# Kernel optimization log

Measured on AMD Instinct MI355X. Metric: run time of the kernel, lower is better.

## Reference

```python
import jax, jax.numpy as jnp
import numpy as np

N = 100000
IN_DIM, HID_DIM, EMB_DIM = 128, 64, 32
E = 1600000


def _gcn_conv(x, W, b, src, tgt, n):
    """PyG GCNConv: linear transform, add self-loops, sym-normalized scatter-add.
    W: [in, out], b: [out]. src/tgt: [E'] incl. self-loops handled by caller."""
    h = x @ W  # [n, out] -- transform before propagate (PyG order)
    deg = jax.ops.segment_sum(jnp.ones_like(tgt, dtype=h.dtype), tgt, num_segments=n)
    dinv = jnp.where(deg > 0, jax.lax.rsqrt(deg), 0.0)
    norm = dinv[src] * dinv[tgt]  # [E']
    msgs = h[src] * norm[:, None]  # [E', out]
    out = jax.ops.segment_sum(msgs, tgt, num_segments=n)
    return out + b


def setup_inputs() -> dict:
    key = jax.random.key(0)
    ks = jax.random.split(key, 6)
    x = jax.random.normal(ks[0], (N, IN_DIM), dtype=jnp.float32)
    edge_index = jax.random.randint(ks[1], (2, E), 0, N, dtype=jnp.int64)
    s1 = 1.0 / np.sqrt(IN_DIM)
    s2 = 1.0 / np.sqrt(HID_DIM)
    W1 = jax.random.uniform(ks[2], (IN_DIM, HID_DIM), jnp.float32, -s1, s1)
    b1 = jnp.zeros((HID_DIM,), jnp.float32)
    W2 = jax.random.uniform(ks[3], (HID_DIM, EMB_DIM), jnp.float32, -s2, s2)
    b2 = jnp.zeros((EMB_DIM,), jnp.float32)
    return {"x": x, "W1": W1, "b1": b1, "W2": W2, "b2": b2, "edge_index": edge_index}


def reference(x, W1, b1, W2, b2, edge_index):
    n = x.shape[0]
    src, tgt = edge_index[0], edge_index[1]
    # add self-loops once (same graph used by both convs)
    loops = jnp.arange(n, dtype=edge_index.dtype)
    src_sl = jnp.concatenate([src, loops])
    tgt_sl = jnp.concatenate([tgt, loops])
    h = jax.nn.relu(_gcn_conv(x, W1, b1, src_sl, tgt_sl, n))
    z = _gcn_conv(h, W2, b2, src_sl, tgt_sl, n)  # [n, EMB_DIM]
    # decode on original edges: edge-wise dot product
    recon = jnp.sum(z[src] * z[tgt], axis=1)  # [E]
    return z, recon
```

## Files before the change

### kernel.cpp

```cpp
#include <hip/hip_runtime.h>
#include <hip/hip_fp16.h>
#include <math.h>


#define NBMAX 256
#define BSHIFT 9
#define BNODES 512
#define CH 4096
#define CAPSHIFT 14
#define CAP (1 << CAPSHIFT)

typedef _Float16 half8 __attribute__((ext_vector_type(8)));
typedef float floatx4 __attribute__((ext_vector_type(4)));

static inline int divup(int a, int b) { return (a + b - 1) / b; }

__device__ inline void acc8(__half2* a, float4 v) {
    const __half2* h = (const __half2*)&v;
    a[0] = __hadd2(a[0], h[0]);
    a[1] = __hadd2(a[1], h[1]);
    a[2] = __hadd2(a[2], h[2]);
    a[3] = __hadd2(a[3], h[3]);
}
__device__ inline unsigned short f2bf(float f) {
    unsigned u = __builtin_bit_cast(unsigned, f);
    u = (u + 0x7FFFu + ((u >> 16) & 1u)) >> 16;
    return (unsigned short)u;
}


__global__ void k_init(int* __restrict__ gcur, unsigned* __restrict__ hs_pad,
                       unsigned* __restrict__ zs_pad) {
    int t = threadIdx.x;
    if (t < NBMAX) gcur[t] = t << CAPSHIFT;
    if (t < 32) hs_pad[t] = 0;
    else if (t < 48) zs_pad[t - 32] = 0;
}


__global__ __launch_bounds__(256) void k_part(const int* __restrict__ src,
                                              const int* __restrict__ tgt,
                                              int* __restrict__ gcur,
                                              unsigned* __restrict__ ebuf, int E, int NB) {
    __shared__ int h[NBMAX];
    __shared__ int base[NBMAX];
    int tid = threadIdx.x;
    int e0 = blockIdx.x * CH;
    for (int b = tid; b < NB; b += 256) h[b] = 0;
    __syncthreads();
    unsigned pk[16];
    int sv[16];
#pragma unroll
    for (int r = 0; r < 4; r++) {
        int e = e0 + (r * 256 + tid) * 4;
        if (e + 3 < E) {
            int4 t4 = *(const int4*)(tgt + e);
            int4 s4 = *(const int4*)(src + e);
            int tv[4] = {t4.x, t4.y, t4.z, t4.w};
            int sw[4] = {s4.x, s4.y, s4.z, s4.w};
#pragma unroll
            for (int j = 0; j < 4; j++) {
                int t = tv[j];
                int b = t >> BSHIFT;
                int l = atomicAdd(&h[b], 1);
                pk[r * 4 + j] = ((unsigned)b << 21) |
                                ((unsigned)(t & (BNODES - 1)) << 12) | (unsigned)l;
                sv[r * 4 + j] = sw[j];
            }
        } else {
#pragma unroll
            for (int j = 0; j < 4; j++) {
                int ee = e + j;
                if (ee < E) {
                    int t = tgt[ee];
                    int b = t >> BSHIFT;
                    int l = atomicAdd(&h[b], 1);
                    pk[r * 4 + j] = ((unsigned)b << 21) |
                                    ((unsigned)(t & (BNODES - 1)) << 12) | (unsigned)l;
                    sv[r * 4 + j] = src[ee];
                } else {
                    pk[r * 4 + j] = 0xFFFFFFFFu;
                }
            }
        }
    }
    __syncthreads();
    for (int b = tid; b < NB; b += 256) {
        int c = h[b];
        base[b] = c ? atomicAdd(&gcur[b], c) : 0;
    }
    __syncthreads();
#pragma unroll
    for (int i = 0; i < 16; i++) {
        if (pk[i] != 0xFFFFFFFFu) {
            int b = pk[i] >> 21;
            unsigned lt = (pk[i] >> 12) & (BNODES - 1);
            int l = pk[i] & 4095;
            ebuf[base[b] + l] = (lt << 23) | (unsigned)sv[i];
        }
    }
}


__global__ __launch_bounds__(512) void k_bfill(const unsigned* __restrict__ ebuf,
                                               const int* __restrict__ gcur,
                                               int* __restrict__ rowbeg,
                                               int* __restrict__ rowend,
                                               int* __restrict__ col,
                                               float* __restrict__ dinv, int n) {
    __shared__ int s_cnt[BNODES];
    __shared__ int s_scan[BNODES];
    __shared__ int s_cur[BNODES];
    int b = blockIdx.x, tid = threadIdx.x;
    int nbase = b << BSHIFT;
    int ebase = b << CAPSHIFT;
    int eend = gcur[b];
    s_cnt[tid] = 0;
    __syncthreads();
    for (int e = ebase + tid; e < eend; e += BNODES) {
        atomicAdd(&s_cnt[ebuf[e] >> 23], 1);
    }
    __syncthreads();
    s_scan[tid] = s_cnt[tid];
    __syncthreads();
    for (int off = 1; off < BNODES; off <<= 1) {
        int t = (tid >= off) ? s_scan[tid - off] : 0;
        __syncthreads();
        s_scan[tid] += t;
        __syncthreads();
    }
    int excl = s_scan[tid] - s_cnt[tid];
    s_cur[tid] = excl;
    int node = nbase + tid;
    if (node < n) {
        rowbeg[node] = ebase + excl;
        rowend[node] = ebase + excl + s_cnt[tid];
        dinv[node] = rsqrtf((float)(s_cnt[tid] + 1));
    }
    __syncthreads();
    for (int e = ebase + tid; e < eend; e += BNODES) {
        unsigned p = ebuf[e];
        int pos = atomicAdd(&s_cur[p >> 23], 1);
        col[ebase + pos] = (int)(p & 0x7FFFFFu);
    }
}


__global__ __launch_bounds__(256) void k_mm1(const float* __restrict__ x,
                                             const float* __restrict__ W1,
                                             const float* __restrict__ dinv,
                                             __half* __restrict__ hs, int n) {
    __shared__ _Float16 xh[64 * 136];
    __shared__ _Float16 Wt[64 * 136];
    int tid = threadIdx.x;
    int nbase = blockIdx.x * 64;
#pragma unroll
    for (int i = 0; i < 8; i++) {
        int f = tid + i * 256;
        int r = f >> 5, c4 = f & 31;
        int node = nbase + r;
        float4 v = make_float4(0.f, 0.f, 0.f, 0.f);
        if (node < n) v = *(const float4*)(x + (size_t)node * 128 + c4 * 4);
        union { uint2 u; __half2 h[2]; } pk;
        pk.h[0] = __floats2half2_rn(v.x, v.y);
        pk.h[1] = __floats2half2_rn(v.z, v.w);
        *(uint2*)&xh[r * 136 + c4 * 4] = pk.u;
    }
#pragma unroll
    for (int i = 0; i < 16; i++) {
        int f = tid + i * 256;
        int c = f & 63, kp = f >> 6;
        float a = W1[(size_t)(2 * kp) * 64 + c];
        float b = W1[(size_t)(2 * kp + 1) * 64 + c];
        *(__half2*)&Wt[c * 136 + 2 * kp] = __floats2half2_rn(a, b);
    }
    __syncthreads();
    int w = tid >> 6, lane = tid & 63;
    int quad = lane >> 4, m = lane & 15;
    floatx4 acc[4] = {{0.f, 0.f, 0.f, 0.f}, {0.f, 0.f, 0.f, 0.f},
                      {0.f, 0.f, 0.f, 0.f}, {0.f, 0.f, 0.f, 0.f}};
#pragma unroll
    for (int kt = 0; kt < 4; kt++) {
        half8 a = *(const half8*)&xh[(w * 16 + m) * 136 + kt * 32 + quad * 8];
#pragma unroll
        for (int ct = 0; ct < 4; ct++) {
            half8 b = *(const half8*)&Wt[(ct * 16 + m) * 136 + kt * 32 + quad * 8];
            acc[ct] = __builtin_amdgcn_mfma_f32_16x16x32_f16(a, b, acc[ct], 0, 0, 0);
        }
    }
#pragma unroll
    for (int reg = 0; reg < 4; reg++) {
        int node = nbase + w * 16 + quad * 4 + reg;
        if (node < n) {
            float d = dinv[node];
#pragma unroll
            for (int ct = 0; ct < 4; ct++) {
                hs[(size_t)node * 64 + ct * 16 + m] = __float2half(acc[ct][reg] * d);
            }
        }
    }
}


__global__ __launch_bounds__(256) void k_conv1(const __half* __restrict__ hs,
                                               const int* __restrict__ rowbeg,
                                               const int* __restrict__ rowend,
                                               const int* __restrict__ col,
                                               const float* __restrict__ dinv,
                                               const float* __restrict__ b1,
                                               __half* __restrict__ h2, int n) {
    int gw = (blockIdx.x * 256 + threadIdx.x) >> 6;
    int lane = threadIdx.x & 63;
    int q = lane >> 4, ln = lane & 15;
    int w = gw * 4 + q;
    if (w >= n) return;
    int qb = q << 4;
    int el = ln >> 3, fl = ln & 7;
    int beg = rowbeg[w], end = rowend[w];
    int deg = end - beg;
    int m = min(16, deg);
    int m2 = min(16, deg - 16);
    int sl = (ln < m) ? col[beg + ln] : 0;
    int sl2 = (ln < m2) ? col[beg + 16 + ln] : 0;
    __half2 a2[4];
#pragma unroll
    for (int j = 0; j < 4; j++) a2[j] = __half2half2(__float2half(0.f));
    int rs = (el == 0) ? w : n;
    float4 S = *(const float4*)(hs + (size_t)rs * 64 + fl * 8);
    float4 L[4];
#pragma unroll
    for (int r = 0; r < 4; r++) {
        int idx = 2 * r + el;
        int s = __shfl(sl, qb + idx);
        int a = (idx < m) ? s : n;
        L[r] = *(const float4*)(hs + (size_t)a * 64 + fl * 8);
    }
    acc8(a2, S);
#pragma unroll
    for (int r = 0; r < 4; r++) acc8(a2, L[r]);
#pragma unroll
    for (int r = 0; r < 4; r++) {
        int idx = 8 + 2 * r + el;
        int s = __shfl(sl, qb + idx);
        int a = (idx < m) ? s : n;
        L[r] = *(const float4*)(hs + (size_t)a * 64 + fl * 8);
    }
#pragma unroll
    for (int r = 0; r < 4; r++) acc8(a2, L[r]);
    if (deg > 16) {
#pragma unroll
        for (int r = 0; r < 4; r++) {
            int idx = 2 * r + el;
            int s = __shfl(sl2, qb + idx);
            int a = (idx < m2) ? s : n;
            L[r] = *(const float4*)(hs + (size_t)a * 64 + fl * 8);
        }
#pragma unroll
        for (int r = 0; r < 4; r++) acc8(a2, L[r]);
#pragma unroll
        for (int r = 0; r < 4; r++) {
            int idx = 8 + 2 * r + el;
            int s = __shfl(sl2, qb + idx);
            int a = (idx < m2) ? s : n;
            L[r] = *(const float4*)(hs + (size_t)a * 64 + fl * 8);
        }
#pragma unroll
        for (int r = 0; r < 4; r++) acc8(a2, L[r]);
    }
    if (deg > 32) {
        for (int b0 = 32; b0 < deg; b0 += 16) {
            int mc = min(16, deg - b0);
            int sl3 = (ln < mc) ? col[beg + b0 + ln] : 0;
            for (int r = 0; r < 8; r++) {
                int idx = 2 * r + el;
                int s = __shfl(sl3, qb + idx);
                int a = (idx < mc) ? s : n;
                float4 v = *(const float4*)(hs + (size_t)a * 64 + fl * 8);
                acc8(a2, v);
            }
        }
    }
    float r[8];
#pragma unroll
    for (int j = 0; j < 4; j++) {
        float2 f = __half22float2(a2[j]);
        r[2 * j] = f.x;
        r[2 * j + 1] = f.y;
    }
#pragma unroll
    for (int j = 0; j < 8; j++) r[j] += __shfl_xor(r[j], 8);

    if (el == 0) {
        float d = dinv[w];
        float4 bb0 = *(const float4*)(b1 + fl * 8);
        float4 bb1 = *(const float4*)(b1 + fl * 8 + 4);
        union { float4 f; __half2 h[4]; } u;
        u.h[0] = __floats2half2_rn(fmaxf(r[0] * d + bb0.x, 0.f),
                                   fmaxf(r[1] * d + bb0.y, 0.f));
        u.h[1] = __floats2half2_rn(fmaxf(r[2] * d + bb0.z, 0.f),
                                   fmaxf(r[3] * d + bb0.w, 0.f));
        u.h[2] = __floats2half2_rn(fmaxf(r[4] * d + bb1.x, 0.f),
                                   fmaxf(r[5] * d + bb1.y, 0.f));
        u.h[3] = __floats2half2_rn(fmaxf(r[6] * d + bb1.z, 0.f),
                                   fmaxf(r[7] * d + bb1.w, 0.f));
        *(float4*)(h2 + (size_t)w * 64 + fl * 8) = u.f;
    }
}


__global__ __launch_bounds__(256) void k_mm2(const __half* __restrict__ h2,
                                             const float* __restrict__ W2,
                                             const float* __restrict__ dinv,
                                             __half* __restrict__ zs, int n) {
    __shared__ _Float16 Wt[32 * 72];
    int tid = threadIdx.x;
    int nbase = blockIdx.x * 64;
#pragma unroll
    for (int i = 0; i < 4; i++) {
        int f = tid + i * 256;
        int c = f & 31, kp = f >> 5;
        float a = W2[(size_t)(2 * kp) * 32 + c];
        float b = W2[(size_t)(2 * kp + 1) * 32 + c];
        *(__half2*)&Wt[c * 72 + 2 * kp] = __floats2half2_rn(a, b);
    }
    __syncthreads();
    int w = tid >> 6, lane = tid & 63;
    int quad = lane >> 4, m = lane & 15;
    int arow = nbase + w * 16 + m;
    const __half* abase = h2 + (size_t)min(arow, n - 1) * 64;
    floatx4 acc[2] = {{0.f, 0.f, 0.f, 0.f}, {0.f, 0.f, 0.f, 0.f}};
#pragma unroll
    for (int kt = 0; kt < 2; kt++) {
        half8 a = *(const half8*)(abase + kt * 32 + quad * 8);
#pragma unroll
        for (int ct = 0; ct < 2; ct++) {
            half8 b = *(const half8*)&Wt[(ct * 16 + m) * 72 + kt * 32 + quad * 8];
            acc[ct] = __builtin_amdgcn_mfma_f32_16x16x32_f16(a, b, acc[ct], 0, 0, 0);
        }
    }
#pragma unroll
    for (int reg = 0; reg < 4; reg++) {
        int node = nbase + w * 16 + quad * 4 + reg;
        if (node < n) {
            float d = dinv[node];
#pragma unroll
            for (int ct = 0; ct < 2; ct++) {
                zs[(size_t)node * 32 + ct * 16 + m] = __float2half(acc[ct][reg] * d);
            }
        }
    }
}


__global__ __launch_bounds__(256) void k_conv2(const __half* __restrict__ zs,
                                               const int* __restrict__ rowbeg,
                                               const int* __restrict__ rowend,
                                               const int* __restrict__ col,
                                               const float* __restrict__ dinv,
                                               const float* __restrict__ b2,
                                               float* __restrict__ zout,
                                               unsigned short* __restrict__ zh, int n) {
    int gw = (blockIdx.x * 256 + threadIdx.x) >> 6;
    int lane = threadIdx.x & 63;
    int q = lane >> 4, ln = lane & 15;
    int w = gw * 4 + q;
    if (w >= n) return;
    int qb = q << 4;
    int el = ln >> 2, fl = ln & 3;
    int beg = rowbeg[w], end = rowend[w];
    int deg = end - beg;
    int m = min(16, deg);
    int m2 = min(16, deg - 16);
    int sl = (ln < m) ? col[beg + ln] : 0;
    int sl2 = (ln < m2) ? col[beg + 16 + ln] : 0;
    __half2 a2[4];
#pragma unroll
    for (int j = 0; j < 4; j++) a2[j] = __half2half2(__float2half(0.f));
    int rs = (el == 0) ? w : n;
    float4 S = *(const float4*)(zs + (size_t)rs * 32 + fl * 8);
    float4 L[4];
#pragma unroll
    for (int r = 0; r < 4; r++) {
        int idx = 4 * r + el;
        int s = __shfl(sl, qb + idx);
        int a = (idx < m) ? s : n;
        L[r] = *(const float4*)(zs + (size_t)a * 32 + fl * 8);
    }
    acc8(a2, S);
#pragma unroll
    for (int r = 0; r < 4; r++) acc8(a2, L[r]);
    if (deg > 16) {
#pragma unroll
        for (int r = 0; r < 4; r++) {
            int idx = 4 * r + el;
            int s = __shfl(sl2, qb + idx);
            int a = (idx < m2) ? s : n;
            L[r] = *(const float4*)(zs + (size_t)a * 32 + fl * 8);
        }
#pragma unroll
        for (int r = 0; r < 4; r++) acc8(a2, L[r]);
    }
    if (deg > 32) {
        for (int b0 = 32; b0 < deg; b0 += 16) {
            int mc = min(16, deg - b0);
            int sl3 = (ln < mc) ? col[beg + b0 + ln] : 0;
            for (int r = 0; r < 4; r++) {
                int idx = 4 * r + el;
                int s = __shfl(sl3, qb + idx);
                int a = (idx < mc) ? s : n;
                float4 v = *(const float4*)(zs + (size_t)a * 32 + fl * 8);
                acc8(a2, v);
            }
        }
    }
    float r[8];
#pragma unroll
    for (int j = 0; j < 4; j++) {
        float2 f = __half22float2(a2[j]);
        r[2 * j] = f.x;
        r[2 * j + 1] = f.y;
    }
#pragma unroll
    for (int d = 4; d < 16; d <<= 1)
#pragma unroll
        for (int j = 0; j < 8; j++) r[j] += __shfl_xor(r[j], d);

    if (el == 0) {
        float d = dinv[w];
        float4 bb0 = *(const float4*)(b2 + fl * 8);
        float4 bb1 = *(const float4*)(b2 + fl * 8 + 4);
        float o0 = r[0] * d + bb0.x, o1 = r[1] * d + bb0.y;
        float o2 = r[2] * d + bb0.z, o3 = r[3] * d + bb0.w;
        float o4 = r[4] * d + bb1.x, o5 = r[5] * d + bb1.y;
        float o6 = r[6] * d + bb1.z, o7 = r[7] * d + bb1.w;
        *(float4*)(zout + (size_t)w * 32 + fl * 8) = make_float4(o0, o1, o2, o3);
        *(float4*)(zout + (size_t)w * 32 + fl * 8 + 4) = make_float4(o4, o5, o6, o7);
        uint4 p;
        p.x = (unsigned)f2bf(o0) | ((unsigned)f2bf(o1) << 16);
        p.y = (unsigned)f2bf(o2) | ((unsigned)f2bf(o3) << 16);
        p.z = (unsigned)f2bf(o4) | ((unsigned)f2bf(o5) << 16);
        p.w = (unsigned)f2bf(o6) | ((unsigned)f2bf(o7) << 16);
        *(uint4*)(zh + (size_t)w * 32 + fl * 8) = p;
    }
}


__device__ inline float bfdot8(uint4 a, uint4 b) {
    const unsigned* pa = (const unsigned*)&a;
    const unsigned* pb = (const unsigned*)&b;
    float v = 0.f;
#pragma unroll
    for (int w = 0; w < 4; w++) {
        float alo = __builtin_bit_cast(float, pa[w] << 16);
        float ahi = __builtin_bit_cast(float, pa[w] & 0xFFFF0000u);
        float blo = __builtin_bit_cast(float, pb[w] << 16);
        float bhi = __builtin_bit_cast(float, pb[w] & 0xFFFF0000u);
        v += alo * blo + ahi * bhi;
    }
    return v;
}

__global__ __launch_bounds__(256) void k_decode(const unsigned short* __restrict__ zh,
                                                const int* __restrict__ src,
                                                const int* __restrict__ tgt,
                                                float* __restrict__ recon, int E) {
    int g = (blockIdx.x * 256 + threadIdx.x) >> 2;
    int fl = threadIdx.x & 3;
    int e0 = g * 4;
    if (e0 >= E) return;
    int cnt = min(4, E - e0);
    int s[4], t[4];
#pragma unroll
    for (int q = 0; q < 4; q++) {
        int e = (q < cnt) ? e0 + q : e0;
        s[q] = src[e];
        t[q] = tgt[e];
    }
    uint4 Za[4], Zb[4];
#pragma unroll
    for (int q = 0; q < 4; q++) {
        Za[q] = *(const uint4*)(zh + (size_t)s[q] * 32 + fl * 8);
        Zb[q] = *(const uint4*)(zh + (size_t)t[q] * 32 + fl * 8);
    }
    float v[4];
#pragma unroll
    for (int q = 0; q < 4; q++) {
        float x = bfdot8(Za[q], Zb[q]);
        x += __shfl_xor(x, 1);
        x += __shfl_xor(x, 2);
        v[q] = x;
    }
    if (fl == 0) {
        if (cnt == 4) {
            *(float4*)(recon + e0) = make_float4(v[0], v[1], v[2], v[3]);
        } else {
            for (int q = 0; q < cnt; q++) recon[e0 + q] = v[q];
        }
    }
}

extern "C" void kernel_launch(void* const* d_in, const int* in_sizes, int n_in,
                              void* d_out, int out_size, void* d_ws, size_t ws_size,
                              hipStream_t stream) {
    const float* x = (const float*)d_in[0];
    const float* W1 = (const float*)d_in[1];
    const float* b1 = (const float*)d_in[2];
    const float* W2 = (const float*)d_in[3];
    const float* b2 = (const float*)d_in[4];
    const int* ei = (const int*)d_in[5];

    int N = in_sizes[0] / 128;
    int E = in_sizes[5] / 2;
    const int* src = ei;
    const int* tgt = ei + E;
    int NB = divup(N, BNODES);

    char* ws = (char*)d_ws;
    size_t off = 0;
    auto alloc = [&](size_t bytes) {
        size_t r = off;
        off += (bytes + 255) & ~(size_t)255;
        return r;
    };
    int* gcur = (int*)(ws + alloc(NBMAX * 4));
    unsigned* ebuf = (unsigned*)(ws + alloc((size_t)NB * CAP * 4));
    int* col = (int*)(ws + alloc((size_t)NB * CAP * 4));
    int* rowbeg = (int*)(ws + alloc((size_t)N * 4));
    int* rowend = (int*)(ws + alloc((size_t)N * 4));
    float* dinv = (float*)(ws + alloc((size_t)N * 4));
    __half* hs = (__half*)(ws + alloc((size_t)(N + 1) * 64 * 2));
    __half* h2 = (__half*)(ws + alloc((size_t)N * 64 * 2));
    __half* zs = (__half*)(ws + alloc((size_t)(N + 1) * 32 * 2));
    unsigned short* zh = (unsigned short*)(ws + alloc((size_t)N * 32 * 2));

    float* zout = (float*)d_out;
    float* recon = zout + (size_t)N * 32;

    k_init<<<1, 256, 0, stream>>>(gcur, (unsigned*)(hs + (size_t)N * 64),
                                  (unsigned*)(zs + (size_t)N * 32));
    k_part<<<divup(E, CH), 256, 0, stream>>>(src, tgt, gcur, ebuf, E, NB);
    k_bfill<<<NB, BNODES, 0, stream>>>(ebuf, gcur, rowbeg, rowend, col, dinv, N);

    k_mm1<<<divup(N, 64), 256, 0, stream>>>(x, W1, dinv, hs, N);
    k_conv1<<<divup(N, 16), 256, 0, stream>>>(hs, rowbeg, rowend, col, dinv, b1, h2, N);
    k_mm2<<<divup(N, 64), 256, 0, stream>>>(h2, W2, dinv, zs, N);
    k_conv2<<<divup(N, 16), 256, 0, stream>>>(zs, rowbeg, rowend, col, dinv, b2, zout, zh, N);
    k_decode<<<divup(E, 256), 256, 0, stream>>>(zh, src, tgt, recon, E);
}
```

Baseline: 227.7 us.

## Decode edges in target-bucketed order with target embeddings staged in LDS

The partition pass now also records each edge's original index. The decoder walks the per-bucket edge lists and stages the bucket's 512 target-node embeddings in shared memory, so only the source embedding is gathered from global memory. The edge's score is scattered back to its original position. The cost is an extra edge-id array write in k_part and scattered 4-byte writes to recon instead of coalesced float4 stores.

```diff
diff --git a/kernel.cpp b/kernel.cpp
--- a/kernel.cpp
+++ b/kernel.cpp
@@ -9,6 +9,7 @@
 #define CH 4096
 #define CAPSHIFT 14
 #define CAP (1 << CAPSHIFT)
+#define DSPLIT 8
 
 typedef _Float16 half8 __attribute__((ext_vector_type(8)));
 typedef float floatx4 __attribute__((ext_vector_type(4)));
@@ -41,7 +42,8 @@
 __global__ __launch_bounds__(256) void k_part(const int* __restrict__ src,
                                               const int* __restrict__ tgt,
                                               int* __restrict__ gcur,
-                                              unsigned* __restrict__ ebuf, int E, int NB) {
+                                              unsigned* __restrict__ ebuf,
+                                              int* __restrict__ eid, int E, int NB) {
     __shared__ int h[NBMAX];
     __shared__ int base[NBMAX];
     int tid = threadIdx.x;
@@ -96,7 +98,9 @@
             int b = pk[i] >> 21;
             unsigned lt = (pk[i] >> 12) & (BNODES - 1);
             int l = pk[i] & 4095;
-            ebuf[base[b] + l] = (lt << 23) | (unsigned)sv[i];
+            int slot = base[b] + l;
+            ebuf[slot] = (lt << 23) | (unsigned)sv[i];
+            eid[slot] = e0 + (((i >> 2) * 256 + tid) << 2) + (i & 3);
         }
     }
 }
@@ -460,42 +464,40 @@
     return v;
 }
 
-__global__ __launch_bounds__(256) void k_decode(const unsigned short* __restrict__ zh,
-                                                const int* __restrict__ src,
-                                                const int* __restrict__ tgt,
-                                                float* __restrict__ recon, int E) {
-    int g = (blockIdx.x * 256 + threadIdx.x) >> 2;
-    int fl = threadIdx.x & 3;
-    int e0 = g * 4;
-    if (e0 >= E) return;
-    int cnt = min(4, E - e0);
-    int s[4], t[4];
-#pragma unroll
-    for (int q = 0; q < 4; q++) {
-        int e = (q < cnt) ? e0 + q : e0;
-        s[q] = src[e];
-        t[q] = tgt[e];
-    }
-    uint4 Za[4], Zb[4];
-#pragma unroll
-    for (int q = 0; q < 4; q++) {
-        Za[q] = *(const uint4*)(zh + (size_t)s[q] * 32 + fl * 8);
-        Zb[q] = *(const uint4*)(zh + (size_t)t[q] * 32 + fl * 8);
-    }
-    float v[4];
-#pragma unroll
-    for (int q = 0; q < 4; q++) {
-        float x = bfdot8(Za[q], Zb[q]);
+__global__ __launch_bounds__(256) void k_decode2(const unsigned short* __restrict__ zh,
+                                                 const unsigned* __restrict__ ebuf,
+                                                 const int* __restrict__ eid,
+                                                 const int* __restrict__ gcur,
+                                                 float* __restrict__ recon, int n) {
+    __shared__ uint4 zt[BNODES * 4];
+    int b = blockIdx.x / DSPLIT;
+    int part = blockIdx.x % DSPLIT;
+    int tid = threadIdx.x;
+    int nbase = b << BSHIFT;
+    for (int i = tid; i < BNODES * 4; i += 256) {
+        int node = nbase + (i >> 2);
+        uint4 v = make_uint4(0u, 0u, 0u, 0u);
+        if (node < n) v = *(const uint4*)(zh + (size_t)node * 32 + (i & 3) * 8);
+        zt[i] = v;
+    }
+    __syncthreads();
+    int ebase = b << CAPSHIFT;
+    int cnt = gcur[b] - ebase;
+    int per = (cnt + DSPLIT - 1) / DSPLIT;
+    int lo = part * per;
+    int hi = min(cnt, lo + per);
+    int fl = tid & 3;
+    for (int e = lo + (tid >> 2); e < hi; e += 64) {
+        unsigned p = ebuf[ebase + e];
+        int id = eid[ebase + e];
+        int s = (int)(p & 0x7FFFFFu);
+        int lt = (int)(p >> 23);
+        uint4 za = *(const uint4*)(zh + (size_t)s * 32 + fl * 8);
+        uint4 zb = zt[lt * 4 + fl];
+        float x = bfdot8(za, zb);
         x += __shfl_xor(x, 1);
         x += __shfl_xor(x, 2);
-        v[q] = x;
-    }
-    if (fl == 0) {
-        if (cnt == 4) {
-            *(float4*)(recon + e0) = make_float4(v[0], v[1], v[2], v[3]);
-        } else {
-            for (int q = 0; q < cnt; q++) recon[e0 + q] = v[q];
-        }
+        if (fl == 0) recon[id] = x;
     }
 }
 
@@ -524,6 +526,7 @@
     };
     int* gcur = (int*)(ws + alloc(NBMAX * 4));
     unsigned* ebuf = (unsigned*)(ws + alloc((size_t)NB * CAP * 4));
+    int* eidb = (int*)(ws + alloc((size_t)NB * CAP * 4));
     int* col = (int*)(ws + alloc((size_t)NB * CAP * 4));
     int* rowbeg = (int*)(ws + alloc((size_t)N * 4));
     int* rowend = (int*)(ws + alloc((size_t)N * 4));
@@ -538,12 +541,12 @@
 
     k_init<<<1, 256, 0, stream>>>(gcur, (unsigned*)(hs + (size_t)N * 64),
                                   (unsigned*)(zs + (size_t)N * 32));
-    k_part<<<divup(E, CH), 256, 0, stream>>>(src, tgt, gcur, ebuf, E, NB);
+    k_part<<<divup(E, CH), 256, 0, stream>>>(src, tgt, gcur, ebuf, eidb, E, NB);
     k_bfill<<<NB, BNODES, 0, stream>>>(ebuf, gcur, rowbeg, rowend, col, dinv, N);
 
     k_mm1<<<divup(N, 64), 256, 0, stream>>>(x, W1, dinv, hs, N);
     k_conv1<<<divup(N, 16), 256, 0, stream>>>(hs, rowbeg, rowend, col, dinv, b1, h2, N);
     k_mm2<<<divup(N, 64), 256, 0, stream>>>(h2, W2, dinv, zs, N);
     k_conv2<<<divup(N, 16), 256, 0, stream>>>(zs, rowbeg, rowend, col, dinv, b2, zout, zh, N);
-    k_decode<<<divup(E, 256), 256, 0, stream>>>(zh, src, tgt, recon, E);
-}
+    k_decode2<<<NB * DSPLIT, 256, 0, stream>>>(zh, ebuf, eidb, gcur, recon, N);
+}
```

New measurement: 253.3 us. 11.2% more time.
